# Performance work log

Hardware: AMD Instinct MI355X
Metric: run time of the kernel (lower is better)

The kernel has to match this reference:

```python
import jax, jax.numpy as jnp
import numpy as np
from jax import lax

B, T = 16384, 1000


def setup_inputs() -> dict:
    key = jax.random.key(0)
    k1, k2, k3, k4 = jax.random.split(key, 4)
    xicovs = jax.random.normal(k1, (B, T, 2, 2), dtype=jnp.float32) * 0.1
    dy = jax.random.normal(k2, (B, T, 2), dtype=jnp.float32) * 0.1
    coeffs_A = jax.random.normal(k3, (2, 2), dtype=jnp.float32) * 0.05
    C = jax.random.normal(k4, (2, 2), dtype=jnp.float32)
    x0 = jnp.zeros((B, 2), dtype=jnp.float32)
    dt = jnp.ones((1,), dtype=jnp.float32) * 0.001
    return {"xicovs": xicovs, "dy": dy, "coeffs_A": coeffs_A, "C": C, "x0": x0, "dt": dt}


def reference(xicovs, dy, coeffs_A, C, x0, dt):
    """Unrolls the GaussianDynamics recurrent cell over T steps with lax.scan.

    Per step (faithful to the original call):
      A_m  = coeffs_A - xicov @ C                     # [B,2,2]
      out  = (C @ x_prev) * dt                        # emitted output
      x    = x_prev + (A_m @ x_prev) * dt + xicov @ dy_t
    Returns (outputs [B,T,2], final_state [B,2]).
    """
    dts = dt[0]

    def step(x, inp):
        xic, dyt = inp  # [B,2,2], [B,2]
        A_m = coeffs_A - jnp.einsum('bij,jk->bik', xic, C)
        out = jnp.einsum('ij,bj->bi', C, x) * dts
        x_new = x + jnp.einsum('bij,bj->bi', A_m, x) * dts + jnp.einsum('bij,bj->bi', xic, dyt)
        return x_new, out

    xs = (jnp.moveaxis(xicovs, 1, 0), jnp.moveaxis(dy, 1, 0))  # time-major
    x_final, outs = lax.scan(step, x0, xs)
    return jnp.moveaxis(outs, 0, 1), x_final
```

## Files before the change

### kernel.cpp

```cpp
#include <hip/hip_runtime.h>


constexpr int BATCH = 16384;
constexpr int TLEN  = 1000;
constexpr int TPB   = 256;
constexpr int SPT   = 4;

typedef float vfloat4 __attribute__((ext_vector_type(4)));
typedef float vfloat2 __attribute__((ext_vector_type(2)));

template <int CTRL, int ROWMASK>
__device__ __forceinline__ float dppf(float oldv, float srcv) {
    return __int_as_float(__builtin_amdgcn_update_dpp(
        __float_as_int(oldv), __float_as_int(srcv), CTRL, ROWMASK, 0xf, false));
}

__global__ __launch_bounds__(TPB, 8) void gd_scan_kernel(
    const float* __restrict__ xicovs,
    const float* __restrict__ dyv,
    const float* __restrict__ cA,
    const float* __restrict__ Cm,
    const float* __restrict__ x0,
    const float* __restrict__ dtp,
    float* __restrict__ out)
{
    __shared__ float s_xi00[TLEN], s_xi01[TLEN], s_xi10[TLEN], s_xi11[TLEN];
    __shared__ float wsum[TPB / 64][6];

    const int b    = blockIdx.x;
    const int tid  = threadIdx.x;
    const int lane = tid & 63;
    const int wv   = tid >> 6;

    const int t0  = tid * SPT;
    const int t0m = (t0 <= TLEN - SPT) ? t0 : (TLEN - SPT);

    const vfloat4* gd4 = reinterpret_cast<const vfloat4*>(dyv + (size_t)b * TLEN * 2);
    const int di = 2 * ((t0m < 0) ? 0 : (t0m >> 1) * (SPT >> 1) / (SPT >> 1));
    const vfloat4 dA = gd4[(t0m >> 1)];
    const vfloat4 dB = gd4[(t0m >> 1) + 1];
    (void)di;

    {
        const vfloat4* gx = reinterpret_cast<const vfloat4*>(xicovs + (size_t)b * TLEN * 4);
        for (int i = tid; i < TLEN; i += TPB) {
            const vfloat4 v = gx[i];
            s_xi00[i] = v.x; s_xi01[i] = v.y; s_xi10[i] = v.z; s_xi11[i] = v.w;
        }
    }

    const float dts = dtp[0];
    const float C00 = Cm[0], C01 = Cm[1], C10 = Cm[2], C11 = Cm[3];
    const float A00 = cA[0], A01 = cA[1], A10 = cA[2], A11 = cA[3];

    __syncthreads();

    const vfloat4 q00 = *reinterpret_cast<const vfloat4*>(&s_xi00[t0m]);
    const vfloat4 q01 = *reinterpret_cast<const vfloat4*>(&s_xi01[t0m]);
    const vfloat4 q10 = *reinterpret_cast<const vfloat4*>(&s_xi10[t0m]);
    const vfloat4 q11 = *reinterpret_cast<const vfloat4*>(&s_xi11[t0m]);

    const float xi00s[SPT] = {q00.x, q00.y, q00.z, q00.w};
    const float xi01s[SPT] = {q01.x, q01.y, q01.z, q01.w};
    const float xi10s[SPT] = {q10.x, q10.y, q10.z, q10.w};
    const float xi11s[SPT] = {q11.x, q11.y, q11.z, q11.w};
    const float dy0s[SPT]  = {dA.x, dA.z, dB.x, dB.z};
    const float dy1s[SPT]  = {dA.y, dA.w, dB.y, dB.w};

    float S00s[SPT], S01s[SPT], S10s[SPT], S11s[SPT], o0s[SPT], o1s[SPT];
    float M00 = 1.f, M01 = 0.f, M10 = 0.f, M11 = 1.f, c0 = 0.f, c1 = 0.f;
#pragma unroll
    for (int s = 0; s < SPT; ++s) {
        const int t = t0 + s;
        const float xi00 = xi00s[s], xi01 = xi01s[s], xi10 = xi10s[s], xi11 = xi11s[s];
        const float Am00 = A00 - (xi00 * C00 + xi01 * C10);
        const float Am01 = A01 - (xi00 * C01 + xi01 * C11);
        const float Am10 = A10 - (xi10 * C00 + xi11 * C10);
        const float Am11 = A11 - (xi10 * C01 + xi11 * C11);
        float S00 = 1.f + Am00 * dts, S01 = Am01 * dts;
        float S10 = Am10 * dts,       S11 = 1.f + Am11 * dts;
        float o0 = xi00 * dy0s[s] + xi01 * dy1s[s];
        float o1 = xi10 * dy0s[s] + xi11 * dy1s[s];
        if (t >= TLEN) { S00 = 1.f; S01 = 0.f; S10 = 0.f; S11 = 1.f; o0 = 0.f; o1 = 0.f; }
        S00s[s] = S00; S01s[s] = S01; S10s[s] = S10; S11s[s] = S11; o0s[s] = o0; o1s[s] = o1;
        const float n00 = S00 * M00 + S01 * M10;
        const float n01 = S00 * M01 + S01 * M11;
        const float n10 = S10 * M00 + S11 * M10;
        const float n11 = S10 * M01 + S11 * M11;
        const float nc0 = S00 * c0 + S01 * c1 + o0;
        const float nc1 = S10 * c0 + S11 * c1 + o1;
        M00 = n00; M01 = n01; M10 = n10; M11 = n11; c0 = nc0; c1 = nc1;
    }

#define SCAN_STEP(CTRL, RM)                                        \
    do {                                                           \
        const float m00 = dppf<CTRL, RM>(1.f, M00);                \
        const float m01 = dppf<CTRL, RM>(0.f, M01);                \
        const float m10 = dppf<CTRL, RM>(0.f, M10);                \
        const float m11 = dppf<CTRL, RM>(1.f, M11);                \
        const float lc0 = dppf<CTRL, RM>(0.f, c0);                 \
        const float lc1 = dppf<CTRL, RM>(0.f, c1);                 \
        const float n00 = M00 * m00 + M01 * m10;                   \
        const float n01 = M00 * m01 + M01 * m11;                   \
        const float n10 = M10 * m00 + M11 * m10;                   \
        const float n11 = M10 * m01 + M11 * m11;                   \
        const float nc0 = M00 * lc0 + M01 * lc1 + c0;              \
        const float nc1 = M10 * lc0 + M11 * lc1 + c1;              \
        M00 = n00; M01 = n01; M10 = n10; M11 = n11;                \
        c0 = nc0; c1 = nc1;                                        \
    } while (0)

    SCAN_STEP(0x111, 0xf);
    SCAN_STEP(0x112, 0xf);
    SCAN_STEP(0x114, 0xf);
    SCAN_STEP(0x118, 0xf);
    SCAN_STEP(0x142, 0xa);
    SCAN_STEP(0x143, 0xc);
#undef SCAN_STEP

    if (lane == 63) {
        wsum[wv][0] = M00; wsum[wv][1] = M01; wsum[wv][2] = M10; wsum[wv][3] = M11;
        wsum[wv][4] = c0;  wsum[wv][5] = c1;
    }
    __syncthreads();

    float P00 = 1.f, P01 = 0.f, P10 = 0.f, P11 = 1.f, Pc0 = 0.f, Pc1 = 0.f;
    for (int w = 0; w < wv; ++w) {
        const float w00 = wsum[w][0], w01 = wsum[w][1], w10 = wsum[w][2], w11 = wsum[w][3];
        const float wc0 = wsum[w][4], wc1 = wsum[w][5];
        const float n00 = w00 * P00 + w01 * P10;
        const float n01 = w00 * P01 + w01 * P11;
        const float n10 = w10 * P00 + w11 * P10;
        const float n11 = w10 * P01 + w11 * P11;
        const float nc0 = w00 * Pc0 + w01 * Pc1 + wc0;
        const float nc1 = w10 * Pc0 + w11 * Pc1 + wc1;
        P00 = n00; P01 = n01; P10 = n10; P11 = n11; Pc0 = nc0; Pc1 = nc1;
    }

    float e00 = __shfl_up(M00, 1), e01 = __shfl_up(M01, 1);
    float e10 = __shfl_up(M10, 1), e11 = __shfl_up(M11, 1);
    float ec0 = __shfl_up(c0, 1),  ec1 = __shfl_up(c1, 1);
    if (lane == 0) { e00 = 1.f; e01 = 0.f; e10 = 0.f; e11 = 1.f; ec0 = 0.f; ec1 = 0.f; }

    const float E00 = e00 * P00 + e01 * P10;
    const float E01 = e00 * P01 + e01 * P11;
    const float E10 = e10 * P00 + e11 * P10;
    const float E11 = e10 * P01 + e11 * P11;
    const float Ec0 = e00 * Pc0 + e01 * Pc1 + ec0;
    const float Ec1 = e10 * Pc0 + e11 * Pc1 + ec1;

    const float xa = x0[2 * b], xb = x0[2 * b + 1];
    float xq0 = E00 * xa + E01 * xb + Ec0;
    float xq1 = E10 * xa + E11 * xb + Ec1;

    float o0v[SPT], o1v[SPT];
#pragma unroll
    for (int s = 0; s < SPT; ++s) {
        o0v[s] = (C00 * xq0 + C01 * xq1) * dts;
        o1v[s] = (C10 * xq0 + C11 * xq1) * dts;
        const float nx0 = S00s[s] * xq0 + S01s[s] * xq1 + o0s[s];
        const float nx1 = S10s[s] * xq0 + S11s[s] * xq1 + o1s[s];
        xq0 = nx0; xq1 = nx1;
    }

    float* ob = out + (size_t)b * TLEN * 2 + (size_t)t0 * 2;
    if (t0 + SPT <= TLEN) {
        vfloat4 w0 = {o0v[0], o1v[0], o0v[1], o1v[1]};
        vfloat4 w1 = {o0v[2], o1v[2], o0v[3], o1v[3]};
        __builtin_nontemporal_store(w0, reinterpret_cast<vfloat4*>(ob));
        __builtin_nontemporal_store(w1, reinterpret_cast<vfloat4*>(ob) + 1);
    } else {
        for (int s = 0; s < SPT; ++s)
            if (t0 + s < TLEN) {
                vfloat2 w = {o0v[s], o1v[s]};
                __builtin_nontemporal_store(w, reinterpret_cast<vfloat2*>(ob) + s);
            }
    }

    if (t0 < TLEN && t0 + SPT >= TLEN) {
        float* xf = out + (size_t)BATCH * TLEN * 2 + 2 * b;
        xf[0] = xq0; xf[1] = xq1;
    }
}

extern "C" void kernel_launch(void* const* d_in, const int* in_sizes, int n_in,
                              void* d_out, int out_size, void* d_ws, size_t ws_size,
                              hipStream_t stream) {
    const float* xicovs = (const float*)d_in[0];
    const float* dyv    = (const float*)d_in[1];
    const float* cA     = (const float*)d_in[2];
    const float* Cm     = (const float*)d_in[3];
    const float* x0     = (const float*)d_in[4];
    const float* dtp    = (const float*)d_in[5];
    float* out = (float*)d_out;

    gd_scan_kernel<<<BATCH, TPB, 0, stream>>>(xicovs, dyv, cA, Cm, x0, dtp, out);
}
```

Before: 100.4 us.

## Load xicovs directly into LDS with wave-local swizzle, fold dt into constants

Replaces the register-staged, de-interleaved shared-memory copy of xicovs with direct global-to-LDS loads (global_load_lds) into a per-wave, XOR-swizzled AoS buffer. Each wave waits only on its own vmcnt instead of a block-wide barrier, then reads its four float4 step records from the swizzled layout. Also pre-scales C and A by dt so the per-step transition and output need fewer multiplies. This relies on each wave loading exactly the slice it consumes. It adds swizzle index arithmetic and a dependence on the LDS-DMA path.

```diff
diff --git a/kernel.cpp b/kernel.cpp
--- a/kernel.cpp
+++ b/kernel.cpp
@@ -24,7 +24,7 @@
     const float* __restrict__ dtp,
     float* __restrict__ out)
 {
-    __shared__ float s_xi00[TLEN], s_xi01[TLEN], s_xi10[TLEN], s_xi11[TLEN];
+    __shared__ vfloat4 s_xc[1024];
     __shared__ float wsum[TPB / 64][6];
 
     const int b    = blockIdx.x;
@@ -35,50 +35,53 @@
     const int t0  = tid * SPT;
     const int t0m = (t0 <= TLEN - SPT) ? t0 : (TLEN - SPT);
 
+    const float* rowx = xicovs + (size_t)b * TLEN * 4;
+
+#pragma unroll
+    for (int k = 0; k < 4; ++k) {
+        const int pw = k * 64 + lane;
+        const int gw = pw ^ ((pw >> 3) & 7);
+        int g = 256 * wv + gw;
+        if (g > TLEN - 1) g = TLEN - 1;
+        __builtin_amdgcn_global_load_lds(
+            (const __attribute__((address_space(1))) void*)(rowx + (size_t)g * 4),
+            (__attribute__((address_space(3))) void*)&s_xc[wv * 256 + k * 64],
+            16, 0, 0);
+    }
+
     const vfloat4* gd4 = reinterpret_cast<const vfloat4*>(dyv + (size_t)b * TLEN * 2);
-    const int di = 2 * ((t0m < 0) ? 0 : (t0m >> 1) * (SPT >> 1) / (SPT >> 1));
     const vfloat4 dA = gd4[(t0m >> 1)];
     const vfloat4 dB = gd4[(t0m >> 1) + 1];
-    (void)di;
-
-    {
-        const vfloat4* gx = reinterpret_cast<const vfloat4*>(xicovs + (size_t)b * TLEN * 4);
-        for (int i = tid; i < TLEN; i += TPB) {
-            const vfloat4 v = gx[i];
-            s_xi00[i] = v.x; s_xi01[i] = v.y; s_xi10[i] = v.z; s_xi11[i] = v.w;
-        }
-    }
 
     const float dts = dtp[0];
-    const float C00 = Cm[0], C01 = Cm[1], C10 = Cm[2], C11 = Cm[3];
-    const float A00 = cA[0], A01 = cA[1], A10 = cA[2], A11 = cA[3];
-
-    __syncthreads();
-
-    const vfloat4 q00 = *reinterpret_cast<const vfloat4*>(&s_xi00[t0m]);
-    const vfloat4 q01 = *reinterpret_cast<const vfloat4*>(&s_xi01[t0m]);
-    const vfloat4 q10 = *reinterpret_cast<const vfloat4*>(&s_xi10[t0m]);
-    const vfloat4 q11 = *reinterpret_cast<const vfloat4*>(&s_xi11[t0m]);
-
-    const float xi00s[SPT] = {q00.x, q00.y, q00.z, q00.w};
-    const float xi01s[SPT] = {q01.x, q01.y, q01.z, q01.w};
-    const float xi10s[SPT] = {q10.x, q10.y, q10.z, q10.w};
-    const float xi11s[SPT] = {q11.x, q11.y, q11.z, q11.w};
-    const float dy0s[SPT]  = {dA.x, dA.z, dB.x, dB.z};
-    const float dy1s[SPT]  = {dA.y, dA.w, dB.y, dB.w};
+    const float Cd00 = Cm[0] * dts, Cd01 = Cm[1] * dts, Cd10 = Cm[2] * dts, Cd11 = Cm[3] * dts;
+    const float nCd00 = -Cd00, nCd01 = -Cd01, nCd10 = -Cd10, nCd11 = -Cd11;
+    const float Ad00 = 1.f + cA[0] * dts, Ad01 = cA[1] * dts;
+    const float Ad10 = cA[2] * dts,       Ad11 = 1.f + cA[3] * dts;
+
+    asm volatile("s_waitcnt vmcnt(0)" ::: "memory");
+
+    vfloat4 xc[SPT];
+#pragma unroll
+    for (int s = 0; s < SPT; ++s) {
+        const int gw  = 4 * lane + s;
+        const int pos = gw ^ ((gw >> 3) & 7);
+        xc[s] = s_xc[wv * 256 + pos];
+    }
+
+    const float dy0s[SPT] = {dA.x, dA.z, dB.x, dB.z};
+    const float dy1s[SPT] = {dA.y, dA.w, dB.y, dB.w};
 
     float S00s[SPT], S01s[SPT], S10s[SPT], S11s[SPT], o0s[SPT], o1s[SPT];
     float M00 = 1.f, M01 = 0.f, M10 = 0.f, M11 = 1.f, c0 = 0.f, c1 = 0.f;
 #pragma unroll
     for (int s = 0; s < SPT; ++s) {
         const int t = t0 + s;
-        const float xi00 = xi00s[s], xi01 = xi01s[s], xi10 = xi10s[s], xi11 = xi11s[s];
-        const float Am00 = A00 - (xi00 * C00 + xi01 * C10);
-        const float Am01 = A01 - (xi00 * C01 + xi01 * C11);
-        const float Am10 = A10 - (xi10 * C00 + xi11 * C10);
-        const float Am11 = A11 - (xi10 * C01 + xi11 * C11);
-        float S00 = 1.f + Am00 * dts, S01 = Am01 * dts;
-        float S10 = Am10 * dts,       S11 = 1.f + Am11 * dts;
+        const float xi00 = xc[s].x, xi01 = xc[s].y, xi10 = xc[s].z, xi11 = xc[s].w;
+        float S00 = Ad00 + xi00 * nCd00 + xi01 * nCd10;
+        float S01 = Ad01 + xi00 * nCd01 + xi01 * nCd11;
+        float S10 = Ad10 + xi10 * nCd00 + xi11 * nCd10;
+        float S11 = Ad11 + xi10 * nCd01 + xi11 * nCd11;
         float o0 = xi00 * dy0s[s] + xi01 * dy1s[s];
         float o1 = xi10 * dy0s[s] + xi11 * dy1s[s];
         if (t >= TLEN) { S00 = 1.f; S01 = 0.f; S10 = 0.f; S11 = 1.f; o0 = 0.f; o1 = 0.f; }
@@ -156,8 +159,8 @@
     float o0v[SPT], o1v[SPT];
 #pragma unroll
     for (int s = 0; s < SPT; ++s) {
-        o0v[s] = (C00 * xq0 + C01 * xq1) * dts;
-        o1v[s] = (C10 * xq0 + C11 * xq1) * dts;
+        o0v[s] = Cd00 * xq0 + Cd01 * xq1;
+        o1v[s] = Cd10 * xq0 + Cd11 * xq1;
         const float nx0 = S00s[s] * xq0 + S01s[s] * xq1 + o0s[s];
         const float nx1 = S10s[s] * xq0 + S11s[s] * xq1 + o1s[s];
         xq0 = nx0; xq1 = nx1;
```

New measurement: 98.81 us. No clear change (-1.6%).
